# Kernel optimization log

Hardware: AMD Instinct MI355X
Metric: run time of the kernel (lower is better)

The kernel has to match this reference:

```python
import jax, jax.numpy as jnp
import numpy as np

POOLED_H = 7
POOLED_W = 7
SPATIAL_SCALE = 0.25
SAMPLING_RATIO = 2


def setup_inputs() -> dict:
    key = jax.random.key(0)
    k1, k2, k3, k4, k5, k6 = jax.random.split(key, 6)
    B, C, H, W = 2, 256, 200, 272
    N = 1000
    feat = jax.random.normal(k1, (B, C, H, W), dtype=jnp.float32)
    img_h = H / SPATIAL_SCALE  # 800
    img_w = W / SPATIAL_SCALE  # 1088
    bidx = jax.random.randint(k2, (N,), 0, B).astype(jnp.float32)
    x1 = jax.random.uniform(k3, (N,)) * (img_w - 64.0)
    y1 = jax.random.uniform(k4, (N,)) * (img_h - 64.0)
    bw = 16.0 + jax.random.uniform(k5, (N,)) * 200.0
    bh = 16.0 + jax.random.uniform(k6, (N,)) * 200.0
    rois = jnp.stack(
        [bidx, x1, y1, jnp.minimum(x1 + bw, img_w - 1.0), jnp.minimum(y1 + bh, img_h - 1.0)],
        axis=1,
    ).astype(jnp.float32)
    return {"feat": feat, "rois": rois}


def _roi_align(feat, rois):
    """Caffe2-style ROIAlign (aligned=False), avg pooling over sampling grid.
    feat: [B, C, H, W], rois: [N, 5] = [batch_ind, x1, y1, x2, y2] (image coords).
    Returns [N, C, POOLED_H, POOLED_W]."""
    B, C, H, W = feat.shape
    sr = SAMPLING_RATIO
    b = rois[:, 0].astype(jnp.int32)                      # [N]
    sw = rois[:, 1] * SPATIAL_SCALE
    sh = rois[:, 2] * SPATIAL_SCALE
    ew = rois[:, 3] * SPATIAL_SCALE
    eh = rois[:, 4] * SPATIAL_SCALE
    roi_w = jnp.maximum(ew - sw, 1.0)
    roi_h = jnp.maximum(eh - sh, 1.0)
    bin_w = roi_w / POOLED_W
    bin_h = roi_h / POOLED_H
    # Flattened sample coords: idx = ph*sr + i  ->  (idx+0.5)/sr = ph + (i+0.5)/sr
    oy = (jnp.arange(POOLED_H * sr, dtype=jnp.float32) + 0.5) / sr  # [Sy]
    ox = (jnp.arange(POOLED_W * sr, dtype=jnp.float32) + 0.5) / sr  # [Sx]
    ys = sh[:, None] + oy[None, :] * bin_h[:, None]                 # [N, Sy]
    xs = sw[:, None] + ox[None, :] * bin_w[:, None]                 # [N, Sx]
    # Out-of-image samples contribute 0 (CUDA kernel semantics: y < -1 or y > H)
    valid_y = (ys > -1.0) & (ys < H)
    valid_x = (xs > -1.0) & (xs < W)
    # Clamp + corner indices
    yc = jnp.clip(ys, 0.0, H - 1.0)
    xc = jnp.clip(xs, 0.0, W - 1.0)
    yl = jnp.floor(yc).astype(jnp.int32)
    xl = jnp.floor(xc).astype(jnp.int32)
    yh = jnp.minimum(yl + 1, H - 1)
    xh = jnp.minimum(xl + 1, W - 1)
    ly = yc - yl.astype(jnp.float32)   # [N, Sy]
    lx = xc - xl.astype(jnp.float32)   # [N, Sx]
    hy = 1.0 - ly
    hx = 1.0 - lx

    def gather(yi, xi):
        # [N, Sy, Sx, C]
        return feat[b[:, None, None], :, yi[:, :, None], xi[:, None, :]]

    val = (
        (hy[:, :, None] * hx[:, None, :])[..., None] * gather(yl, xl)
        + (hy[:, :, None] * lx[:, None, :])[..., None] * gather(yl, xh)
        + (ly[:, :, None] * hx[:, None, :])[..., None] * gather(yh, xl)
        + (ly[:, :, None] * lx[:, None, :])[..., None] * gather(yh, xh)
    )
    val = val * (valid_y[:, :, None] & valid_x[:, None, :])[..., None]
    N = rois.shape[0]
    # Average sr*sr samples per bin
    val = val.reshape(N, POOLED_H, sr, POOLED_W, sr, C).mean(axis=(2, 4))
    return val.transpose(0, 3, 1, 2)  # [N, C, PH, PW]


def reference(feat, rois):
    return _roi_align(feat, rois)
```

## Files before the change

kernel.cpp:

```cpp
#include <hip/hip_runtime.h>

#define PH 7
#define PW 7
#define SR 2
#define SY (PH * SR)
#define SX (PW * SR)
#define CH 256
#define FH 200
#define FW 272
#define BINS (PH * PW)
#define NPIX (FH * FW)

typedef float  floatx4 __attribute__((ext_vector_type(4)));

__device__ __forceinline__ unsigned short f2bf(float f) {
    unsigned x = __float_as_uint(f);
    return (unsigned short)((x + 0x7fffu + ((x >> 16) & 1u)) >> 16);
}
__device__ __forceinline__ float bflo(unsigned u) { return __uint_as_float(u << 16); }
__device__ __forceinline__ float bfhi(unsigned u) { return __uint_as_float(u & 0xffff0000u); }

__global__ __launch_bounds__(256) void transpose_kernel(
    const float* __restrict__ feat, unsigned short* __restrict__ featT) {
    __shared__ __align__(16) unsigned short tile[FW][66];
    const int t  = threadIdx.x;
    const int bh = blockIdx.x;
    const int c0 = blockIdx.y * 64;
    const int b  = bh / FH;
    const int h  = bh % FH;

    const int cl  = t >> 2;
    const int wq0 = t & 3;
    const floatx4* __restrict__ src = (const floatx4*)(
        feat + (size_t)b * CH * NPIX + (size_t)(c0 + cl) * NPIX + (size_t)h * FW);
    #pragma unroll
    for (int k = 0; k < 17; ++k) {
        const int fidx = wq0 + 4 * k;
        const floatx4 v = __builtin_nontemporal_load(src + fidx);
        const int w = fidx * 4;
        tile[w + 0][cl] = f2bf(v.x);
        tile[w + 1][cl] = f2bf(v.y);
        tile[w + 2][cl] = f2bf(v.z);
        tile[w + 3][cl] = f2bf(v.w);
    }
    __syncthreads();

    const int cd = t & 31;
    const int wl = t >> 5;
    unsigned* __restrict__ dstu = (unsigned*)featT;
    const size_t pixbase = (size_t)bh * FW;
    #pragma unroll
    for (int k = 0; k < 34; ++k) {
        const int w = wl + 8 * k;
        const unsigned p = *(const unsigned*)&tile[w][2 * cd];
        dstu[(pixbase + w) * (CH / 2) + (c0 >> 1) + cd] = p;
    }
}

__global__ __launch_bounds__(512) void roialign_cl_kernel(
    const unsigned short* __restrict__ featT,
    const float* __restrict__ rois,
    float* __restrict__ out, int N) {
    __shared__ int   s_yl[SY], s_yh[SY];
    __shared__ float s_ly[SY], s_hy[SY];
    __shared__ int   s_xl[SX], s_xh[SX];
    __shared__ float s_lx[SX], s_hx[SX];
    __shared__ __align__(16) unsigned short s_out16[BINS * CH];

    const int n   = blockIdx.x;
    const int tid = threadIdx.x;
    const float* __restrict__ roi = rois + (size_t)n * 5;

    if (tid < SY + SX) {
        const bool isy = (tid < SY);
        const int  idx = isy ? tid : tid - SY;
        const int  lim = isy ? FH : FW;
        const float start = (isy ? roi[2] : roi[1]) * 0.25f;
        const float end_  = (isy ? roi[4] : roi[3]) * 0.25f;
        const float len   = fmaxf(end_ - start, 1.0f);
        const float binsz = len * (isy ? (1.0f / PH) : (1.0f / PW));
        const float s = start + ((float)idx + 0.5f) * (1.0f / SR) * binsz;
        const float valid = (s > -1.0f && s < (float)lim) ? 0.5f : 0.0f;
        const float cc = fminf(fmaxf(s, 0.0f), (float)(lim - 1));
        const int   lo = (int)floorf(cc);
        const int   hi = min(lo + 1, lim - 1);
        const float l  = (cc - (float)lo) * valid;
        const float hw = (1.0f - (cc - (float)lo)) * valid;
        const int   rowstride = FW * (CH / 2);
        if (isy) { s_yl[idx] = lo * rowstride; s_yh[idx] = hi * rowstride;
                   s_ly[idx] = l; s_hy[idx] = hw; }
        else     { s_xl[idx] = lo * (CH / 2);  s_xh[idx] = hi * (CH / 2);
                   s_lx[idx] = l; s_hx[idx] = hw; }
    }
    __syncthreads();

    const int b  = (int)roi[0];
    const int c8 = tid & 31;
    const int g  = tid >> 5;
    const unsigned* __restrict__ fbu =
        (const unsigned*)featT + (size_t)b * (FH * FW * (CH / 2)) + c8 * 4;

    const int bstart = g * 3;
    const int bend   = (g == 15) ? BINS : bstart + 3;

    #pragma unroll 1
    for (int bin = bstart; bin < bend; ++bin) {
        const int ph = bin / 7;
        const int pw = bin - ph * 7;
        const int sy = ph * SR, sx = pw * SR;
        float a0 = 0.f, a1 = 0.f, a2 = 0.f, a3 = 0.f;
        float a4 = 0.f, a5 = 0.f, a6 = 0.f, a7 = 0.f;
        #pragma unroll
        for (int i = 0; i < SR; ++i) {
            const int   yo0 = s_yl[sy + i], yo1 = s_yh[sy + i];
            const float wy1 = s_ly[sy + i], wy0 = s_hy[sy + i];
            #pragma unroll
            for (int j = 0; j < SR; ++j) {
                const int   xo0 = s_xl[sx + j], xo1 = s_xh[sx + j];
                const float wx1 = s_lx[sx + j], wx0 = s_hx[sx + j];
                const uint4 u00 = *(const uint4*)(fbu + yo0 + xo0);
                const uint4 u01 = *(const uint4*)(fbu + yo0 + xo1);
                const uint4 u10 = *(const uint4*)(fbu + yo1 + xo0);
                const uint4 u11 = *(const uint4*)(fbu + yo1 + xo1);
                const float w00 = wy0 * wx0, w01 = wy0 * wx1;
                const float w10 = wy1 * wx0, w11 = wy1 * wx1;
                a0 += w00 * bflo(u00.x) + w01 * bflo(u01.x) + w10 * bflo(u10.x) + w11 * bflo(u11.x);
                a1 += w00 * bfhi(u00.x) + w01 * bfhi(u01.x) + w10 * bfhi(u10.x) + w11 * bfhi(u11.x);
                a2 += w00 * bflo(u00.y) + w01 * bflo(u01.y) + w10 * bflo(u10.y) + w11 * bflo(u11.y);
                a3 += w00 * bfhi(u00.y) + w01 * bfhi(u01.y) + w10 * bfhi(u10.y) + w11 * bfhi(u11.y);
                a4 += w00 * bflo(u00.z) + w01 * bflo(u01.z) + w10 * bflo(u10.z) + w11 * bflo(u11.z);
                a5 += w00 * bfhi(u00.z) + w01 * bfhi(u01.z) + w10 * bfhi(u10.z) + w11 * bfhi(u11.z);
                a6 += w00 * bflo(u00.w) + w01 * bflo(u01.w) + w10 * bflo(u10.w) + w11 * bflo(u11.w);
                a7 += w00 * bfhi(u00.w) + w01 * bfhi(u01.w) + w10 * bfhi(u10.w) + w11 * bfhi(u11.w);
            }
        }
        uint4 p;
        p.x = (unsigned)f2bf(a0) | ((unsigned)f2bf(a1) << 16);
        p.y = (unsigned)f2bf(a2) | ((unsigned)f2bf(a3) << 16);
        p.z = (unsigned)f2bf(a4) | ((unsigned)f2bf(a5) << 16);
        p.w = (unsigned)f2bf(a6) | ((unsigned)f2bf(a7) << 16);
        const int col = (c8 ^ (bin & 31)) * 8;
        *(uint4*)&s_out16[bin * CH + col] = p;
    }
    __syncthreads();

    float* __restrict__ outn = out + (size_t)n * (CH * BINS);
    #pragma unroll 1
    for (int k = 0; k < 24; ++k) {
        const int e   = k * 512 + tid;
        const int c   = e / 49;
        const int bin = e - c * 49;
        const int oct = (c >> 3) ^ (bin & 31);
        __builtin_nontemporal_store(
            bflo((unsigned)s_out16[bin * CH + oct * 8 + (c & 7)]), &outn[e]);
    }
    if (tid < 256) {
        const int e   = 12288 + tid;
        const int c   = e / 49;
        const int bin = e - c * 49;
        const int oct = (c >> 3) ^ (bin & 31);
        __builtin_nontemporal_store(
            bflo((unsigned)s_out16[bin * CH + oct * 8 + (c & 7)]), &outn[e]);
    }
}

__global__ __launch_bounds__(256) void roialign_kernel(
    const float* __restrict__ feat,
    const float* __restrict__ rois,
    float* __restrict__ out, int N) {
    __shared__ int   s_yl[SY], s_yh[SY];
    __shared__ float s_ly[SY], s_hy[SY];
    __shared__ int   s_xl[SX], s_xh[SX];
    __shared__ float s_lx[SX], s_hx[SX];
    __shared__ float s_out[CH * BINS];

    const int n   = blockIdx.x;
    const int tid = threadIdx.x;
    const float* __restrict__ roi = rois + (size_t)n * 5;

    if (tid < SY + SX) {
        const bool isy = (tid < SY);
        const int  idx = isy ? tid : tid - SY;
        const int  lim = isy ? FH : FW;
        const float start = (isy ? roi[2] : roi[1]) * 0.25f;
        const float end_  = (isy ? roi[4] : roi[3]) * 0.25f;
        const float len   = fmaxf(end_ - start, 1.0f);
        const float binsz = len * (isy ? (1.0f / PH) : (1.0f / PW));
        const float s = start + ((float)idx + 0.5f) * (1.0f / SR) * binsz;
        const float valid = (s > -1.0f && s < (float)lim) ? 1.0f : 0.0f;
        const float cc = fminf(fmaxf(s, 0.0f), (float)(lim - 1));
        const int   lo = (int)floorf(cc);
        const int   hi = min(lo + 1, lim - 1);
        const float l  = (cc - (float)lo) * valid;
        const float hw = (1.0f - (cc - (float)lo)) * valid;
        if (isy) { s_yl[idx] = lo; s_yh[idx] = hi; s_ly[idx] = l; s_hy[idx] = hw; }
        else     { s_xl[idx] = lo; s_xh[idx] = hi; s_lx[idx] = l; s_hx[idx] = hw; }
    }
    __syncthreads();

    const int b = (int)roi[0];
    const int c = tid;
    const float* __restrict__ fp = feat + ((size_t)b * CH + c) * (size_t)NPIX;

    #pragma unroll 1
    for (int ph = 0; ph < PH; ++ph) {
        const int sy0 = ph * SR;
        const float* r00 = fp + s_yl[sy0] * FW;
        const float* r01 = fp + s_yh[sy0] * FW;
        const float* r10 = fp + s_yl[sy0 + 1] * FW;
        const float* r11 = fp + s_yh[sy0 + 1] * FW;
        const float ly0 = s_ly[sy0],     hy0 = s_hy[sy0];
        const float ly1 = s_ly[sy0 + 1], hy1 = s_hy[sy0 + 1];
        for (int pw = 0; pw < PW; ++pw) {
            const int sx0 = pw * SR;
            float acc = 0.0f;
            #pragma unroll
            for (int j = 0; j < SR; ++j) {
                const int   xl = s_xl[sx0 + j], xh = s_xh[sx0 + j];
                const float lx = s_lx[sx0 + j], hx = s_hx[sx0 + j];
                acc += hy0 * (hx * r00[xl] + lx * r00[xh])
                     + ly0 * (hx * r01[xl] + lx * r01[xh]);
                acc += hy1 * (hx * r10[xl] + lx * r10[xh])
                     + ly1 * (hx * r11[xl] + lx * r11[xh]);
            }
            s_out[c * BINS + ph * PW + pw] = acc * 0.25f;
        }
    }
    __syncthreads();

    float* __restrict__ outn = out + (size_t)n * (CH * BINS);
    #pragma unroll
    for (int k = 0; k < BINS; ++k) {
        const int idx = k * 256 + tid;
        outn[idx] = s_out[idx];
    }
}

extern "C" void kernel_launch(void* const* d_in, const int* in_sizes, int n_in,
                              void* d_out, int out_size, void* d_ws, size_t ws_size,
                              hipStream_t stream) {
    const float* feat = (const float*)d_in[0];
    const float* rois = (const float*)d_in[1];
    float* out = (float*)d_out;
    const int N = in_sizes[1] / 5;
    const int B = in_sizes[0] / (CH * NPIX);
    const size_t need = (size_t)B * CH * NPIX * sizeof(unsigned short);

    if (ws_size >= need) {
        unsigned short* featT = (unsigned short*)d_ws;
        dim3 tgrid(B * FH, CH / 64);
        transpose_kernel<<<tgrid, 256, 0, stream>>>(feat, featT);
        roialign_cl_kernel<<<N, 512, 0, stream>>>(featT, rois, out, N);
    } else {
        roialign_kernel<<<N, 256, 0, stream>>>(feat, rois, out, N);
    }
}
```

Before: 220.6 us.

## Reorder ROI blocks by batch and y-band so each XCD shares cached features

Adds a single-block counting-sort kernel that buckets ROIs by batch index and coarse y coordinate. It then assigns the sorted ROIs round-robin so that consecutive sorted ROIs land on the same XCD (block index modulo 8). The ROIAlign kernel reads its ROI index through this permutation, so that spatially nearby ROIs share L2 lines on one XCD and refetch less feature data. The cost is an extra serial launch and a dependent load of the permutation at the start of each block. The mapping also assumes blocks are dispatched round-robin across 8 XCDs.

```diff
diff --git a/kernel.cpp b/kernel.cpp
--- a/kernel.cpp
+++ b/kernel.cpp
@@ -10,6 +10,7 @@
 #define FW 272
 #define BINS (PH * PW)
 #define NPIX (FH * FW)
+#define MAXN 1024
 
 typedef float  floatx4 __attribute__((ext_vector_type(4)));
 
@@ -19,6 +20,49 @@
 }
 __device__ __forceinline__ float bflo(unsigned u) { return __uint_as_float(u << 16); }
 __device__ __forceinline__ float bfhi(unsigned u) { return __uint_as_float(u & 0xffff0000u); }
+
+__global__ __launch_bounds__(MAXN) void sortperm_kernel(
+    const float* __restrict__ rois, int* __restrict__ perm, int N) {
+    const int t = threadIdx.x;
+    if (N > MAXN) {
+        for (int i = t; i < N; i += MAXN) perm[i] = i;
+        return;
+    }
+    __shared__ unsigned short s_key[MAXN];
+    __shared__ int s_scan[256];
+    __shared__ int s_cnt[256];
+    if (t < 256) s_scan[t] = 0;
+    __syncthreads();
+    if (t < N) {
+        const float b = rois[t * 5 + 0];
+        const float y = rois[t * 5 + 2] * 0.25f;
+        int yk = (int)(y * (128.0f / 200.0f));
+        yk = min(127, max(0, yk));
+        const int key = (((int)b) & 1) * 128 + yk;
+        s_key[t] = (unsigned short)key;
+        atomicAdd(&s_scan[key], 1);
+    }
+    __syncthreads();
+    #pragma unroll
+    for (int off = 1; off < 256; off <<= 1) {
+        int v = 0;
+        if (t < 256 && t >= off) v = s_scan[t - off];
+        __syncthreads();
+        if (t < 256) s_scan[t] += v;
+        __syncthreads();
+    }
+    if (t < 256) s_cnt[t] = (t == 0) ? 0 : s_scan[t - 1];
+    __syncthreads();
+    if (t < N) {
+        const int k = s_key[t];
+        const int p = atomicAdd(&s_cnt[k], 1);
+        const int q = N >> 3, r = N & 7;
+        int xcd, j;
+        if (p < r * (q + 1)) { xcd = p / (q + 1); j = p - xcd * (q + 1); }
+        else { const int pp = p - r * (q + 1); xcd = r + pp / q; j = pp - (xcd - r) * q; }
+        perm[8 * j + xcd] = t;
+    }
+}
 
 __global__ __launch_bounds__(256) void transpose_kernel(
     const float* __restrict__ feat, unsigned short* __restrict__ featT) {
@@ -60,6 +104,7 @@
 __global__ __launch_bounds__(512) void roialign_cl_kernel(
     const unsigned short* __restrict__ featT,
     const float* __restrict__ rois,
+    const int* __restrict__ perm,
     float* __restrict__ out, int N) {
     __shared__ int   s_yl[SY], s_yh[SY];
     __shared__ float s_ly[SY], s_hy[SY];
@@ -67,7 +112,7 @@
     __shared__ float s_lx[SX], s_hx[SX];
     __shared__ __align__(16) unsigned short s_out16[BINS * CH];
 
-    const int n   = blockIdx.x;
+    const int n   = perm[blockIdx.x];
     const int tid = threadIdx.x;
     const float* __restrict__ roi = rois + (size_t)n * 5;
 
@@ -244,13 +289,16 @@
     float* out = (float*)d_out;
     const int N = in_sizes[1] / 5;
     const int B = in_sizes[0] / (CH * NPIX);
-    const size_t need = (size_t)B * CH * NPIX * sizeof(unsigned short);
+    const size_t featT_bytes = (size_t)B * CH * NPIX * sizeof(unsigned short);
+    const size_t need = featT_bytes + (size_t)N * sizeof(int);
 
     if (ws_size >= need) {
         unsigned short* featT = (unsigned short*)d_ws;
+        int* perm = (int*)((char*)d_ws + featT_bytes);
+        sortperm_kernel<<<1, MAXN, 0, stream>>>(rois, perm, N);
         dim3 tgrid(B * FH, CH / 64);
         transpose_kernel<<<tgrid, 256, 0, stream>>>(feat, featT);
-        roialign_cl_kernel<<<N, 512, 0, stream>>>(featT, rois, out, N);
+        roialign_cl_kernel<<<N, 512, 0, stream>>>(featT, rois, perm, out, N);
     } else {
         roialign_kernel<<<N, 256, 0, stream>>>(feat, rois, out, N);
     }
```

After: 215.2 us. -2.4%, faster.
